# Performance work log

Hardware: AMD Instinct MI355X
Metric: run time of the kernel (lower is better)

## Reference

```python
import jax, jax.numpy as jnp
import numpy as np

DIM = 2048
HID = 1024
E = 16
TOP_K = 2
S_SHARED = 2


def setup_inputs() -> dict:
    key = jax.random.key(0)
    ks = jax.random.split(key, 6)
    scale = 0.02
    x = jax.random.normal(ks[0], (2, 2048, DIM), dtype=jnp.float32)
    gate_w = jax.random.normal(ks[1], (DIM, E), dtype=jnp.float32) * scale
    shared_w1 = jax.random.normal(ks[2], (S_SHARED, DIM, HID), dtype=jnp.float32) * scale
    shared_w2 = jax.random.normal(ks[3], (S_SHARED, HID, DIM), dtype=jnp.float32) * scale
    w1 = jax.random.normal(ks[4], (E, DIM, HID), dtype=jnp.float32) * scale
    w2 = jax.random.normal(ks[5], (E, HID, DIM), dtype=jnp.float32) * scale
    return {"x": x, "gate_w": gate_w, "shared_w1": shared_w1,
            "shared_w2": shared_w2, "w1": w1, "w2": w2}


def reference(x, gate_w, shared_w1, shared_w2, w1, w2):
    orig_shape = x.shape
    xf = x.reshape(-1, orig_shape[-1])  # [T, D]

    # Shared experts: sum of SiLU MLPs
    hs = jax.nn.silu(jnp.einsum('td,sdh->sth', xf, shared_w1))
    shared_out = jnp.einsum('sth,shd->td', hs, shared_w2)

    # Gating
    probs = jax.nn.softmax(xf @ gate_w, axis=-1)              # [T, E]
    weights, indices = jax.lax.top_k(probs, TOP_K)            # [T, K]
    weights = weights / weights.sum(axis=-1, keepdims=True)
    aux_loss = (probs.mean(axis=0) ** 2).sum() * E

    # Combine weights per (token, expert): top_k indices are distinct
    combine = (jax.nn.one_hot(indices, E, dtype=xf.dtype) *
               weights[..., None]).sum(axis=1)                # [T, E]

    # Dense all-expert compute (reference form of gather-GEMM-scatter)
    h = jax.nn.silu(jnp.einsum('td,edh->eth', xf, w1))        # [E, T, H]
    y = jnp.einsum('eth,ehd->etd', h, w2)                     # [E, T, D]
    routed_out = jnp.einsum('te,etd->td', combine, y)         # [T, D]

    out = (shared_out + routed_out).reshape(orig_shape)
    return out, aux_loss
```

## Files before the change

### kernel.cpp

```cpp
#include <hip/hip_runtime.h>
#include <math.h>

typedef unsigned short u16;
typedef __bf16 bf16x8 __attribute__((ext_vector_type(8)));
typedef float f32x4 __attribute__((ext_vector_type(4)));

#define T_TOK 4096
#define DIMD 2048
#define HIDD 1024
#define NEXP 16
#define RMAX 10240
#define MAXBLK 96
#define BM 128
#define BN 128
#define BK 32

__device__ __forceinline__ u16 f2b(float f) {
  unsigned u = __builtin_bit_cast(unsigned, f);
  unsigned r = (u + 0x7FFFu + ((u >> 16) & 1u)) >> 16;
  return (u16)r;
}

__device__ __forceinline__ void gld16(const void* g, void* l) {
  __builtin_amdgcn_global_load_lds(
      (const __attribute__((address_space(1))) void*)g,
      (__attribute__((address_space(3))) void*)l, 16, 0, 0);
}


__global__ void k_init(int* perm, int* cnt, int* fill) {
  int i = blockIdx.x * blockDim.x + threadIdx.x;
  if (i < RMAX) perm[i] = -1;
  if (i < NEXP) { cnt[i] = 0; fill[i] = 0; }
}

__global__ void k_cvt(const float* __restrict__ x, u16* __restrict__ xb) {
  const int i = blockIdx.x * blockDim.x + threadIdx.x;
  const float4 v = ((const float4*)x)[i];
  union { u16 u[4]; unsigned long long q; } t;
  t.u[0] = f2b(v.x); t.u[1] = f2b(v.y); t.u[2] = f2b(v.z); t.u[3] = f2b(v.w);
  ((unsigned long long*)xb)[i] = t.q;
}

__global__ __launch_bounds__(256)
void k_tr(const float* __restrict__ W, u16* __restrict__ Wt,
          int K, int N, long estride, int ld_out) {
  __shared__ float t[64][65];
  const int e = blockIdx.z;
  const float* Win = W + (size_t)e * (size_t)K * (size_t)N;
  u16* Wo = Wt + (size_t)e * (size_t)estride;
  const int n0 = blockIdx.x * 64, k0 = blockIdx.y * 64;
  const int r = threadIdx.x >> 4;
  const int c = (threadIdx.x & 15) * 4;
#pragma unroll
  for (int p = 0; p < 4; ++p) {
    const int kk = p * 16 + r;
    const float4 v = *(const float4*)&Win[(size_t)(k0 + kk) * N + n0 + c];
    t[kk][c] = v.x; t[kk][c + 1] = v.y; t[kk][c + 2] = v.z; t[kk][c + 3] = v.w;
  }
  __syncthreads();
#pragma unroll
  for (int p = 0; p < 4; ++p) {
    const int nn = p * 16 + r;
    ushort4 o;
    o.x = f2b(t[c + 0][nn]); o.y = f2b(t[c + 1][nn]);
    o.z = f2b(t[c + 2][nn]); o.w = f2b(t[c + 3][nn]);
    *(ushort4*)&Wo[(size_t)(n0 + nn) * ld_out + k0 + c] = o;
  }
}

__global__ __launch_bounds__(256)
void k_gate(const float* __restrict__ x, const float* __restrict__ gw,
            int* __restrict__ top2i, float* __restrict__ top2w,
            int* __restrict__ cnt, float* __restrict__ partial) {
  const int e = threadIdx.x & 15;
  const int tt = threadIdx.x >> 4;
  const int t = blockIdx.x * 16 + tt;
  const float* xp = x + (size_t)t * DIMD;
  float acc = 0.f;
#pragma unroll 8
  for (int k = 0; k < DIMD; ++k) acc = fmaf(xp[k], gw[k * NEXP + e], acc);
  __shared__ float lg[16][17];
  __shared__ float pr[16][17];
  lg[tt][e] = acc;
  __syncthreads();
  if (e == 0) {
    float l[16];
    float mx = -1e30f;
    for (int j = 0; j < 16; ++j) { l[j] = lg[tt][j]; mx = fmaxf(mx, l[j]); }
    float s = 0.f;
    for (int j = 0; j < 16; ++j) { l[j] = expf(l[j] - mx); s += l[j]; }
    const float inv = 1.f / s;
    float p1 = -1.f, p2 = -1.f; int i1 = 0, i2 = 0;
    for (int j = 0; j < 16; ++j) {
      const float p = l[j] * inv;
      pr[tt][j] = p;
      if (p > p1) { p2 = p1; i2 = i1; p1 = p; i1 = j; }
      else if (p > p2) { p2 = p; i2 = j; }
    }
    const float wsum = p1 + p2;
    top2i[t * 2 + 0] = i1;
    top2i[t * 2 + 1] = i2;
    top2w[t * 2 + 0] = p1 / wsum;
    top2w[t * 2 + 1] = p2 / wsum;
    atomicAdd(&cnt[i1], 1);
    atomicAdd(&cnt[i2], 1);
  }
  __syncthreads();
  if (tt == 0) {
    float s = 0.f;
    for (int j = 0; j < 16; ++j) s += pr[j][e];
    partial[blockIdx.x * 16 + e] = s;
  }
}

__global__ __launch_bounds__(256)
void k_aux(const float* __restrict__ partial, float* __restrict__ auxOut) {
  __shared__ float s[16][17];
  const int e = threadIdx.x & 15, c = threadIdx.x >> 4;
  float a = 0.f;
  for (int b = c; b < 256; b += 16) a += partial[b * 16 + e];
  s[c][e] = a;
  __syncthreads();
  if (threadIdx.x == 0) {
    float aux = 0.f;
    for (int j = 0; j < 16; ++j) {
      float tot = 0.f;
      for (int cc = 0; cc < 16; ++cc) tot += s[cc][j];
      const float m = tot / (float)T_TOK;
      aux += m * m;
    }
    auxOut[0] = aux * (float)NEXP;
  }
}

__global__ void k_off(const int* __restrict__ cnt, int* __restrict__ offs,
                      int* __restrict__ tbl_e, int* __restrict__ tbl_r0,
                      int* __restrict__ nblk) {
  if (threadIdx.x != 0 || blockIdx.x != 0) return;
  int o = 0, nb = 0;
  for (int e = 0; e < NEXP; ++e) {
    offs[e] = o;
    const int b = (cnt[e] + BM - 1) / BM;
    for (int i = 0; i < b; ++i) { tbl_e[nb] = e; tbl_r0[nb] = o + i * BM; ++nb; }
    o += b * BM;
  }
  offs[NEXP] = o;
  nblk[0] = nb;
}

__global__ void k_fill(const int* __restrict__ top2i, const float* __restrict__ top2w,
                       const int* __restrict__ offs, int* __restrict__ fill,
                       int* __restrict__ perm, float* __restrict__ wrow) {
  const int id = blockIdx.x * blockDim.x + threadIdx.x;
  if (id >= T_TOK * 2) return;
  const int e = top2i[id];
  const int pos = atomicAdd(&fill[e], 1);
  const int r = offs[e] + pos;
  perm[r] = id >> 1;
  wrow[r] = top2w[id];
}

template<int MODE>
__global__ __launch_bounds__(256)
void k_gemm(const u16* __restrict__ A, const u16* __restrict__ Bt,
            void* __restrict__ Outp,
            const int* __restrict__ perm, const float* __restrict__ wrow,
            const int* __restrict__ tbl_e, const int* __restrict__ tbl_r0,
            const int* __restrict__ nblk,
            int K, int lda, int ldb, size_t bstride) {
  __shared__ u16 As[BM * BK];
  __shared__ u16 Bs[BN * BK];

  const int bx = blockIdx.x, by = blockIdx.y;
  int expert = 0, r0;
  if (MODE == 2 || MODE == 3) {
    if (bx >= *nblk) return;
    expert = tbl_e[bx];
    r0 = tbl_r0[bx];
  } else {
    r0 = bx * BM;
    if (MODE == 0) expert = blockIdx.z;
  }
  const u16* B = Bt + (size_t)expert * bstride;

  const int tid = threadIdx.x;
  const int w = tid >> 6, lane = tid & 63;
  const int lr = lane >> 2;
  const int lk = (lane & 3) * 8;

  int ra0 = r0 + w * 32 + lr, ra1 = ra0 + 16;
  if (MODE == 2) {
    const int p0 = perm[ra0]; ra0 = (p0 < 0) ? 0 : p0;
    const int p1 = perm[ra1]; ra1 = (p1 < 0) ? 0 : p1;
  }
  const int n0 = by * BN;
  const u16* ap0 = A + (size_t)ra0 * lda + lk;
  const u16* ap1 = A + (size_t)ra1 * lda + lk;
  const u16* bp0 = B + (size_t)(n0 + w * 32 + lr) * ldb + lk;
  const u16* bp1 = bp0 + (size_t)16 * ldb;
  u16* lA0 = &As[w * 1024];
  u16* lA1 = &As[w * 1024 + 512];
  u16* lB0 = &Bs[w * 1024];
  u16* lB1 = &Bs[w * 1024 + 512];

  f32x4 acc[4][4];
#pragma unroll
  for (int i = 0; i < 4; ++i)
#pragma unroll
    for (int j = 0; j < 4; ++j) {
      acc[i][j][0] = 0.f; acc[i][j][1] = 0.f; acc[i][j][2] = 0.f; acc[i][j][3] = 0.f;
    }

  const int wr = (w >> 1) * 64, wc = (w & 1) * 64;
  const int lm = lane & 15, lq = lane >> 4;
  const u16* aRd = &As[(wr + lm) * BK + lq * 8];
  const u16* bRd = &Bs[(wc + lm) * BK + lq * 8];

  for (int k0 = 0; k0 < K; k0 += BK) {
    gld16(ap0 + k0, lA0);
    gld16(ap1 + k0, lA1);
    gld16(bp0 + k0, lB0);
    gld16(bp1 + k0, lB1);
    __syncthreads();
    bf16x8 af[4], bq[4];
#pragma unroll
    for (int i = 0; i < 4; ++i) af[i] = *(const bf16x8*)(aRd + i * 16 * BK);
#pragma unroll
    for (int j = 0; j < 4; ++j) bq[j] = *(const bf16x8*)(bRd + j * 16 * BK);
#pragma unroll
    for (int i = 0; i < 4; ++i)
#pragma unroll
      for (int j = 0; j < 4; ++j)
        acc[i][j] = __builtin_amdgcn_mfma_f32_16x16x32_bf16(af[i], bq[j], acc[i][j], 0, 0, 0);
    __syncthreads();
  }

  u16* outB16 = (u16*)Outp;
  float* outF = (float*)Outp;
#pragma unroll
  for (int i = 0; i < 4; ++i) {
    const int lr0 = wr + i * 16 + lq * 4;
#pragma unroll
    for (int j = 0; j < 4; ++j) {
      const int gc = n0 + wc + j * 16 + lm;
#pragma unroll
      for (int r = 0; r < 4; ++r) {
        const float v = acc[i][j][r];
        const int lrow = lr0 + r;
        if (MODE == 0) {
          const float s = v / (1.f + expf(-v));
          outB16[(size_t)(r0 + lrow) * DIMD + expert * HIDD + gc] = f2b(s);
        } else if (MODE == 2) {
          const float s = v / (1.f + expf(-v));
          outB16[(size_t)(r0 + lrow) * HIDD + gc] = f2b(s);
        } else if (MODE == 1) {
          outF[(size_t)(r0 + lrow) * DIMD + gc] = v;
        } else {
          const int rr = r0 + lrow;
          const int t = perm[rr];
          if (t >= 0) atomicAdd(&outF[(size_t)t * DIMD + gc], wrow[rr] * v);
        }
      }
    }
  }
}


extern "C" void kernel_launch(void* const* d_in, const int* in_sizes, int n_in,
                              void* d_out, int out_size, void* d_ws, size_t ws_size,
                              hipStream_t stream) {
  const float* x   = (const float*)d_in[0];
  const float* gw  = (const float*)d_in[1];
  const float* sw1 = (const float*)d_in[2];
  const float* sw2 = (const float*)d_in[3];
  const float* w1  = (const float*)d_in[4];
  const float* w2  = (const float*)d_in[5];
  float* out = (float*)d_out;

  char* ws = (char*)d_ws;
  u16* xb    = (u16*)(ws);
  u16* hbS   = (u16*)(ws + (size_t)( 16 << 20));
  u16* hbR   = (u16*)(ws + (size_t)( 32 << 20));
  u16* sw1t  = (u16*)(ws + (size_t)( 52 << 20));
  u16* sw2ct = (u16*)(ws + (size_t)( 60 << 20));
  u16* w1t   = (u16*)(ws + (size_t)( 68 << 20));
  u16* w2t   = (u16*)(ws + (size_t)(132 << 20));
  char* p = ws + (size_t)(196 << 20);
  int*   top2i   = (int*)p;    p += T_TOK * 2 * 4;
  float* top2w   = (float*)p;  p += T_TOK * 2 * 4;
  int*   perm    = (int*)p;    p += RMAX * 4;
  float* wrow    = (float*)p;  p += RMAX * 4;
  int*   cnt     = (int*)p;    p += 16 * 4;
  int*   fill    = (int*)p;    p += 16 * 4;
  int*   offs    = (int*)p;    p += 32 * 4;
  int*   tbl_e   = (int*)p;    p += MAXBLK * 4;
  int*   tbl_r0  = (int*)p;    p += MAXBLK * 4;
  int*   nblk    = (int*)p;    p += 16 * 4;
  float* partial = (float*)p;  p += 256 * 16 * 4;

  k_init<<<(RMAX + 255) / 256, 256, 0, stream>>>(perm, cnt, fill);
  k_cvt<<<(T_TOK * DIMD / 4) / 256, 256, 0, stream>>>(x, xb);
  k_gate<<<T_TOK / 16, 256, 0, stream>>>(x, gw, top2i, top2w, cnt, partial);
  k_off<<<1, 64, 0, stream>>>(cnt, offs, tbl_e, tbl_r0, nblk);
  k_fill<<<(T_TOK * 2 + 255) / 256, 256, 0, stream>>>(top2i, top2w, offs, fill, perm, wrow);
  k_aux<<<1, 256, 0, stream>>>(partial, out + (size_t)T_TOK * DIMD);

  k_tr<<<dim3(1024 / 64, 2048 / 64,  2), 256, 0, stream>>>(sw1, sw1t, 2048, 1024, 1024l * 2048, 2048);
  k_tr<<<dim3(2048 / 64, 1024 / 64,  2), 256, 0, stream>>>(sw2, sw2ct, 1024, 2048, 1024, 2048);
  k_tr<<<dim3(1024 / 64, 2048 / 64, 16), 256, 0, stream>>>(w1, w1t, 2048, 1024, 1024l * 2048, 2048);
  k_tr<<<dim3(2048 / 64, 1024 / 64, 16), 256, 0, stream>>>(w2, w2t, 1024, 2048, 2048l * 1024, 1024);

  k_gemm<0><<<dim3(32, 8, 2), 256, 0, stream>>>(xb, sw1t, hbS,
      nullptr, nullptr, nullptr, nullptr, nullptr, 2048, 2048, 2048, (size_t)1024 * 2048);
  k_gemm<1><<<dim3(32, 16, 1), 256, 0, stream>>>(hbS, sw2ct, out,
      nullptr, nullptr, nullptr, nullptr, nullptr, 2048, 2048, 2048, 0);
  k_gemm<2><<<dim3(80, 8, 1), 256, 0, stream>>>(xb, w1t, hbR,
      perm, nullptr, tbl_e, tbl_r0, nblk, 2048, 2048, 2048, (size_t)1024 * 2048);
  k_gemm<3><<<dim3(80, 16, 1), 256, 0, stream>>>(hbR, w2t, out,
      perm, wrow, tbl_e, tbl_r0, nblk, 1024, 1024, 1024, (size_t)2048 * 1024);
}
```

Measured before the change: 858.3 us.

## Merge shared and routed GEMMs into grouped launches, swizzle LDS, replace atomics

Shared-expert and routed-expert GEMMs now share a single grouped launch per phase, driven by block tables, so each phase fills the GPU with one dispatch. The K tile grows from 32 to 64, and LDS uses an XOR swizzle to avoid bank conflicts. Routed down-projection outputs are written as bf16 per top-k slot instead of fp32 atomicAdd, and a new combine kernel sums them into the output. This removes atomic contention and launch gaps, at the cost of an extra pass over a bf16 buffer and added bf16 rounding of routed contributions.

```diff
diff --git a/kernel.cpp b/kernel.cpp
--- a/kernel.cpp
+++ b/kernel.cpp
@@ -10,17 +10,16 @@
 #define HIDD 1024
 #define NEXP 16
 #define RMAX 10240
-#define MAXBLK 96
-#define BM 128
-#define BN 128
-#define BK 32
+#define MAXBLK 160
 
 __device__ __forceinline__ u16 f2b(float f) {
   unsigned u = __builtin_bit_cast(unsigned, f);
   unsigned r = (u + 0x7FFFu + ((u >> 16) & 1u)) >> 16;
   return (u16)r;
 }
-
+__device__ __forceinline__ float b2f(u16 u) {
+  return __builtin_bit_cast(float, (unsigned)u << 16);
+}
 __device__ __forceinline__ void gld16(const void* g, void* l) {
   __builtin_amdgcn_global_load_lds(
       (const __attribute__((address_space(1))) void*)g,
@@ -135,23 +134,33 @@
 }
 
 __global__ void k_off(const int* __restrict__ cnt, int* __restrict__ offs,
-                      int* __restrict__ tbl_e, int* __restrict__ tbl_r0,
+                      int* __restrict__ tUe, int* __restrict__ tUr,
+                      int* __restrict__ tDe, int* __restrict__ tDr,
                       int* __restrict__ nblk) {
   if (threadIdx.x != 0 || blockIdx.x != 0) return;
+  for (int s = 0; s < 2; ++s)
+    for (int i = 0; i < 32; ++i) { tUe[s * 32 + i] = 16 + s; tUr[s * 32 + i] = i * 128; }
+  for (int i = 0; i < 32; ++i) { tDe[i] = 16; tDr[i] = i * 128; }
   int o = 0, nb = 0;
   for (int e = 0; e < NEXP; ++e) {
     offs[e] = o;
-    const int b = (cnt[e] + BM - 1) / BM;
-    for (int i = 0; i < b; ++i) { tbl_e[nb] = e; tbl_r0[nb] = o + i * BM; ++nb; }
-    o += b * BM;
+    const int b = (cnt[e] + 127) / 128;
+    for (int i = 0; i < b; ++i) {
+      tUe[64 + nb] = e; tUr[64 + nb] = o + i * 128;
+      tDe[32 + nb] = e; tDr[32 + nb] = o + i * 128;
+      ++nb;
+    }
+    o += b * 128;
   }
   offs[NEXP] = o;
-  nblk[0] = nb;
+  nblk[0] = 64 + nb;
+  nblk[1] = 32 + nb;
 }
 
 __global__ void k_fill(const int* __restrict__ top2i, const float* __restrict__ top2w,
                        const int* __restrict__ offs, int* __restrict__ fill,
-                       int* __restrict__ perm, float* __restrict__ wrow) {
+                       int* __restrict__ perm, float* __restrict__ wrow,
+                       int* __restrict__ slot) {
   const int id = blockIdx.x * blockDim.x + threadIdx.x;
   if (id >= T_TOK * 2) return;
   const int e = top2i[id];
@@ -159,50 +168,59 @@
   const int r = offs[e] + pos;
   perm[r] = id >> 1;
   wrow[r] = top2w[id];
-}
-
-template<int MODE>
-__global__ __launch_bounds__(256)
-void k_gemm(const u16* __restrict__ A, const u16* __restrict__ Bt,
-            void* __restrict__ Outp,
+  slot[r] = id & 1;
+}
+
+template<int PHASE>
+__global__ __launch_bounds__(256)
+void k_gemm(const u16* __restrict__ Ar, const u16* __restrict__ Ash,
+            const u16* __restrict__ Wr, const u16* __restrict__ Wsh,
+            void* __restrict__ oR, void* __restrict__ oS,
             const int* __restrict__ perm, const float* __restrict__ wrow,
-            const int* __restrict__ tbl_e, const int* __restrict__ tbl_r0,
-            const int* __restrict__ nblk,
-            int K, int lda, int ldb, size_t bstride) {
-  __shared__ u16 As[BM * BK];
-  __shared__ u16 Bs[BN * BK];
+            const int* __restrict__ slot,
+            const int* __restrict__ te, const int* __restrict__ tr,
+            const int* __restrict__ nblk) {
+  __shared__ u16 LA[128 * 64];
+  __shared__ u16 LB[128 * 64];
+  __shared__ int rowS[128];
 
   const int bx = blockIdx.x, by = blockIdx.y;
-  int expert = 0, r0;
-  if (MODE == 2 || MODE == 3) {
-    if (bx >= *nblk) return;
-    expert = tbl_e[bx];
-    r0 = tbl_r0[bx];
+  if (bx >= nblk[PHASE]) return;
+  const int e = te[bx];
+  const int r0 = tr[bx];
+  const bool sh = (e >= 16);
+
+  const u16* A; const u16* B; int lda, K, ldb;
+  if (PHASE == 0) {
+    A = Ar; lda = 2048; K = 2048; ldb = 2048;
+    B = sh ? (Wsh + (size_t)(e - 16) * (1024 * 2048))
+           : (Wr + (size_t)e * (1024 * 2048));
   } else {
-    r0 = bx * BM;
-    if (MODE == 0) expert = blockIdx.z;
-  }
-  const u16* B = Bt + (size_t)expert * bstride;
+    if (sh) { A = Ash; lda = 2048; K = 2048; ldb = 2048; B = Wsh; }
+    else    { A = Ar;  lda = 1024; K = 1024; ldb = 1024; B = Wr + (size_t)e * (2048 * 1024); }
+  }
 
   const int tid = threadIdx.x;
+  if (tid < 128) {
+    int v;
+    if (PHASE == 0 && !sh) { const int p = perm[r0 + tid]; v = (p < 0) ? 0 : p; }
+    else v = r0 + tid;
+    rowS[tid] = v;
+  }
+  __syncthreads();
+
   const int w = tid >> 6, lane = tid & 63;
-  const int lr = lane >> 2;
-  const int lk = (lane & 3) * 8;
-
-  int ra0 = r0 + w * 32 + lr, ra1 = ra0 + 16;
-  if (MODE == 2) {
-    const int p0 = perm[ra0]; ra0 = (p0 < 0) ? 0 : p0;
-    const int p1 = perm[ra1]; ra1 = (p1 < 0) ? 0 : p1;
-  }
-  const int n0 = by * BN;
-  const u16* ap0 = A + (size_t)ra0 * lda + lk;
-  const u16* ap1 = A + (size_t)ra1 * lda + lk;
-  const u16* bp0 = B + (size_t)(n0 + w * 32 + lr) * ldb + lk;
-  const u16* bp1 = bp0 + (size_t)16 * ldb;
-  u16* lA0 = &As[w * 1024];
-  u16* lA1 = &As[w * 1024 + 512];
-  u16* lB0 = &Bs[w * 1024];
-  u16* lB1 = &Bs[w * 1024 + 512];
+  const int sr = lane >> 3;
+  const int sc = lane & 7;
+  const int kx = (sc ^ sr) << 3;
+  const u16* ap[4];
+#pragma unroll
+  for (int i = 0; i < 4; ++i)
+    ap[i] = A + (size_t)rowS[w * 32 + i * 8 + sr] * lda + kx;
+  const int n0 = by * 128;
+  const u16* bp = B + (size_t)(n0 + w * 32 + sr) * ldb + kx;
+  u16* la = &LA[w * 32 * 64];
+  u16* lb = &LB[w * 32 * 64];
 
   f32x4 acc[4][4];
 #pragma unroll
@@ -214,30 +232,34 @@
 
   const int wr = (w >> 1) * 64, wc = (w & 1) * 64;
   const int lm = lane & 15, lq = lane >> 4;
-  const u16* aRd = &As[(wr + lm) * BK + lq * 8];
-  const u16* bRd = &Bs[(wc + lm) * BK + lq * 8];
-
-  for (int k0 = 0; k0 < K; k0 += BK) {
-    gld16(ap0 + k0, lA0);
-    gld16(ap1 + k0, lA1);
-    gld16(bp0 + k0, lB0);
-    gld16(bp1 + k0, lB1);
+  const int c0 = lq ^ (lm & 7);
+  const int aO = (wr + lm) * 64;
+  const int bO = (wc + lm) * 64;
+
+  for (int k0 = 0; k0 < K; k0 += 64) {
+#pragma unroll
+    for (int i = 0; i < 4; ++i) {
+      gld16(ap[i] + k0, la + i * 512);
+      gld16(bp + (size_t)i * 8 * ldb + k0, lb + i * 512);
+    }
     __syncthreads();
-    bf16x8 af[4], bq[4];
-#pragma unroll
-    for (int i = 0; i < 4; ++i) af[i] = *(const bf16x8*)(aRd + i * 16 * BK);
-#pragma unroll
-    for (int j = 0; j < 4; ++j) bq[j] = *(const bf16x8*)(bRd + j * 16 * BK);
-#pragma unroll
-    for (int i = 0; i < 4; ++i)
-#pragma unroll
-      for (int j = 0; j < 4; ++j)
-        acc[i][j] = __builtin_amdgcn_mfma_f32_16x16x32_bf16(af[i], bq[j], acc[i][j], 0, 0, 0);
+#pragma unroll
+    for (int h = 0; h < 2; ++h) {
+      const int cc = (h ? (c0 ^ 4) : c0) << 3;
+      bf16x8 af[4], bq[4];
+#pragma unroll
+      for (int i = 0; i < 4; ++i) af[i] = *(const bf16x8*)&LA[aO + cc + i * 1024];
+#pragma unroll
+      for (int j = 0; j < 4; ++j) bq[j] = *(const bf16x8*)&LB[bO + cc + j * 1024];
+#pragma unroll
+      for (int i = 0; i < 4; ++i)
+#pragma unroll
+        for (int j = 0; j < 4; ++j)
+          acc[i][j] = __builtin_amdgcn_mfma_f32_16x16x32_bf16(af[i], bq[j], acc[i][j], 0, 0, 0);
+    }
     __syncthreads();
   }
 
-  u16* outB16 = (u16*)Outp;
-  float* outF = (float*)Outp;
 #pragma unroll
   for (int i = 0; i < 4; ++i) {
     const int lr0 = wr + i * 16 + lq * 4;
@@ -248,22 +270,48 @@
       for (int r = 0; r < 4; ++r) {
         const float v = acc[i][j][r];
         const int lrow = lr0 + r;
-        if (MODE == 0) {
-          const float s = v / (1.f + expf(-v));
-          outB16[(size_t)(r0 + lrow) * DIMD + expert * HIDD + gc] = f2b(s);
-        } else if (MODE == 2) {
-          const float s = v / (1.f + expf(-v));
-          outB16[(size_t)(r0 + lrow) * HIDD + gc] = f2b(s);
-        } else if (MODE == 1) {
-          outF[(size_t)(r0 + lrow) * DIMD + gc] = v;
+        if (PHASE == 0) {
+          const float sv = v / (1.f + expf(-v));
+          if (!sh) ((u16*)oR)[(size_t)(r0 + lrow) * HIDD + gc] = f2b(sv);
+          else ((u16*)oS)[(size_t)(r0 + lrow) * DIMD + (e - 16) * HIDD + gc] = f2b(sv);
         } else {
-          const int rr = r0 + lrow;
-          const int t = perm[rr];
-          if (t >= 0) atomicAdd(&outF[(size_t)t * DIMD + gc], wrow[rr] * v);
+          if (sh) {
+            ((float*)oS)[(size_t)(r0 + lrow) * DIMD + gc] = v;
+          } else {
+            const int rr = r0 + lrow;
+            const int t = perm[rr];
+            if (t >= 0)
+              ((u16*)oR)[((size_t)t * 2 + slot[rr]) * DIMD + gc] = f2b(wrow[rr] * v);
+          }
         }
       }
     }
   }
+}
+
+__global__ __launch_bounds__(256)
+void k_comb(float* __restrict__ out, const u16* __restrict__ y) {
+  const int t = blockIdx.x;
+  const int d = threadIdx.x * 8;
+  const size_t b0 = (size_t)(t * 2) * DIMD + d;
+  const size_t b1 = (size_t)(t * 2 + 1) * DIMD + d;
+  ushort4 y0a = *(const ushort4*)&y[b0];
+  ushort4 y0b = *(const ushort4*)&y[b0 + 4];
+  ushort4 y1a = *(const ushort4*)&y[b1];
+  ushort4 y1b = *(const ushort4*)&y[b1 + 4];
+  float* op = out + (size_t)t * DIMD + d;
+  float4 o0 = *(float4*)op;
+  float4 o1 = *(float4*)(op + 4);
+  o0.x += b2f(y0a.x) + b2f(y1a.x);
+  o0.y += b2f(y0a.y) + b2f(y1a.y);
+  o0.z += b2f(y0a.z) + b2f(y1a.z);
+  o0.w += b2f(y0a.w) + b2f(y1a.w);
+  o1.x += b2f(y0b.x) + b2f(y1b.x);
+  o1.y += b2f(y0b.y) + b2f(y1b.y);
+  o1.z += b2f(y0b.z) + b2f(y1b.z);
+  o1.w += b2f(y0b.w) + b2f(y1b.w);
+  *(float4*)op = o0;
+  *(float4*)(op + 4) = o1;
 }
 
 
@@ -282,28 +330,32 @@
   u16* xb    = (u16*)(ws);
   u16* hbS   = (u16*)(ws + (size_t)( 16 << 20));
   u16* hbR   = (u16*)(ws + (size_t)( 32 << 20));
-  u16* sw1t  = (u16*)(ws + (size_t)( 52 << 20));
-  u16* sw2ct = (u16*)(ws + (size_t)( 60 << 20));
-  u16* w1t   = (u16*)(ws + (size_t)( 68 << 20));
-  u16* w2t   = (u16*)(ws + (size_t)(132 << 20));
-  char* p = ws + (size_t)(196 << 20);
+  u16* y     = (u16*)(ws + (size_t)( 52 << 20));
+  u16* sw1t  = (u16*)(ws + (size_t)( 84 << 20));
+  u16* sw2ct = (u16*)(ws + (size_t)( 92 << 20));
+  u16* w1t   = (u16*)(ws + (size_t)(100 << 20));
+  u16* w2t   = (u16*)(ws + (size_t)(164 << 20));
+  char* p = ws + (size_t)(228 << 20);
   int*   top2i   = (int*)p;    p += T_TOK * 2 * 4;
   float* top2w   = (float*)p;  p += T_TOK * 2 * 4;
   int*   perm    = (int*)p;    p += RMAX * 4;
   float* wrow    = (float*)p;  p += RMAX * 4;
+  int*   slot    = (int*)p;    p += RMAX * 4;
   int*   cnt     = (int*)p;    p += 16 * 4;
   int*   fill    = (int*)p;    p += 16 * 4;
   int*   offs    = (int*)p;    p += 32 * 4;
-  int*   tbl_e   = (int*)p;    p += MAXBLK * 4;
-  int*   tbl_r0  = (int*)p;    p += MAXBLK * 4;
+  int*   tUe     = (int*)p;    p += MAXBLK * 4;
+  int*   tUr     = (int*)p;    p += MAXBLK * 4;
+  int*   tDe     = (int*)p;    p += MAXBLK * 4;
+  int*   tDr     = (int*)p;    p += MAXBLK * 4;
   int*   nblk    = (int*)p;    p += 16 * 4;
   float* partial = (float*)p;  p += 256 * 16 * 4;
 
   k_init<<<(RMAX + 255) / 256, 256, 0, stream>>>(perm, cnt, fill);
   k_cvt<<<(T_TOK * DIMD / 4) / 256, 256, 0, stream>>>(x, xb);
   k_gate<<<T_TOK / 16, 256, 0, stream>>>(x, gw, top2i, top2w, cnt, partial);
-  k_off<<<1, 64, 0, stream>>>(cnt, offs, tbl_e, tbl_r0, nblk);
-  k_fill<<<(T_TOK * 2 + 255) / 256, 256, 0, stream>>>(top2i, top2w, offs, fill, perm, wrow);
+  k_off<<<1, 64, 0, stream>>>(cnt, offs, tUe, tUr, tDe, tDr, nblk);
+  k_fill<<<(T_TOK * 2 + 255) / 256, 256, 0, stream>>>(top2i, top2w, offs, fill, perm, wrow, slot);
   k_aux<<<1, 256, 0, stream>>>(partial, out + (size_t)T_TOK * DIMD);
 
   k_tr<<<dim3(1024 / 64, 2048 / 64,  2), 256, 0, stream>>>(sw1, sw1t, 2048, 1024, 1024l * 2048, 2048);
@@ -311,12 +363,9 @@
   k_tr<<<dim3(1024 / 64, 2048 / 64, 16), 256, 0, stream>>>(w1, w1t, 2048, 1024, 1024l * 2048, 2048);
   k_tr<<<dim3(2048 / 64, 1024 / 64, 16), 256, 0, stream>>>(w2, w2t, 1024, 2048, 2048l * 1024, 1024);
 
-  k_gemm<0><<<dim3(32, 8, 2), 256, 0, stream>>>(xb, sw1t, hbS,
-      nullptr, nullptr, nullptr, nullptr, nullptr, 2048, 2048, 2048, (size_t)1024 * 2048);
-  k_gemm<1><<<dim3(32, 16, 1), 256, 0, stream>>>(hbS, sw2ct, out,
-      nullptr, nullptr, nullptr, nullptr, nullptr, 2048, 2048, 2048, 0);
-  k_gemm<2><<<dim3(80, 8, 1), 256, 0, stream>>>(xb, w1t, hbR,
-      perm, nullptr, tbl_e, tbl_r0, nblk, 2048, 2048, 2048, (size_t)1024 * 2048);
-  k_gemm<3><<<dim3(80, 16, 1), 256, 0, stream>>>(hbR, w2t, out,
-      perm, wrow, tbl_e, tbl_r0, nblk, 1024, 1024, 1024, (size_t)2048 * 1024);
-}
+  k_gemm<0><<<dim3(144, 8), 256, 0, stream>>>(xb, xb, w1t, sw1t, hbR, hbS,
+      perm, wrow, slot, tUe, tUr, nblk);
+  k_gemm<1><<<dim3(112, 16), 256, 0, stream>>>(hbR, hbS, w2t, sw2ct, y, out,
+      perm, wrow, slot, tDe, tDr, nblk);
+  k_comb<<<T_TOK, 256, 0, stream>>>(out, y);
+}
```

After: 870.7 us. Within noise of the previous version (+1.4%).
